# Kernel tuning notes

Hardware: AMD Instinct MI355X
Metric: run time of the kernel (lower is better)

## Reference

```python
import jax, jax.numpy as jnp
import numpy as np

DT = 0.1
EPS = 0.01


def _trans_layer(x, W, b):
    # x: [B, 2U]; W: [U, U]; b: [U]
    U = b.shape[0]
    t = DT / EPS
    u_in, v_in = x[:, :U], x[:, U:]
    act = jnp.tanh(u_in)
    v_star = (v_in + t * act) / (1.0 + t)
    # Block matrix A = [[I, dt*W], [-dt*W^T, I]] -- identical for all samples,
    # so factor/solve ONCE with a multi-RHS solve instead of torch's per-sample batched LU.
    I = jnp.eye(U, dtype=x.dtype)
    A = jnp.block([[I, DT * W], [-DT * W.T, I]])  # [2U, 2U]
    rhs = jnp.concatenate([u_in + DT * b, v_star], axis=1)  # [B, 2U]
    y = jnp.linalg.solve(A, rhs.T).T  # [B, 2U]
    u, v = y[:, :U], y[:, U:]
    u_out = DT * (v @ W.T) - u_in - DT * b
    v_out = -DT * (u @ W) + t * v - v_in - t * act
    return jnp.concatenate([u_out, v_out], axis=1)


def setup_inputs() -> dict:
    key = jax.random.key(0)
    ks = jax.random.split(key, 14)
    B, D_IN, U, D_OUT = 32768, 256, 256, 10

    def lin_w(k, o, i):
        return (jax.random.uniform(k, (o, i), jnp.float32) * 2.0 - 1.0) / np.sqrt(i).astype(np.float32)

    def lin_b(k, o, fan_in):
        return (jax.random.uniform(k, (o,), jnp.float32) * 2.0 - 1.0) / np.sqrt(fan_in).astype(np.float32)

    return {
        'x': jax.random.normal(ks[0], (B, D_IN), jnp.float32),
        'Wi': lin_w(ks[1], U, D_IN), 'bi': lin_b(ks[2], U, D_IN),
        'W1': lin_w(ks[3], U, U), 'b1': lin_b(ks[4], U, U),
        'W2': lin_w(ks[5], U, U), 'b2': lin_b(ks[6], U, U),
        'W3': lin_w(ks[7], U, U), 'b3': lin_b(ks[8], U, U),
        'W4': lin_w(ks[9], U, U), 'b4': lin_b(ks[10], U, U),
        'Wo': lin_w(ks[11], D_OUT, U), 'bo': lin_b(ks[12], D_OUT, U),
    }


def reference(x, Wi, bi, W1, b1, W2, b2, W3, b3, W4, b4, Wo, bo):
    U = W1.shape[0]
    z = x @ Wi.T + bi                       # linearInput
    z = jnp.concatenate([z, jnp.tanh(z)], axis=1)  # [B, 2U]
    for W, b in ((W1, b1), (W2, b2), (W3, b3), (W4, b4)):
        z = _trans_layer(z, W, b)
    z = z[:, :U]
    logits = z @ Wo.T + bo                  # linearOutput
    return jax.nn.softmax(logits, axis=1)
```

## Files before the change

### kernel.cpp

```cpp
#include <hip/hip_runtime.h>
#include <math.h>

#define DTC 0.1f

typedef _Float16 half8 __attribute__((ext_vector_type(8)));
typedef _Float16 half4v __attribute__((ext_vector_type(4)));
typedef float f32x4 __attribute__((ext_vector_type(4)));

__device__ __forceinline__ float fast_tanh(float x) {
  const float e = __expf(2.f * x);
  const float r = __builtin_amdgcn_rcpf(e + 1.f);
  return fmaf(-2.f, r, 1.f);
}


__global__ __launch_bounds__(256) void k_prep(
    const float* __restrict__ W0, const float* __restrict__ W1,
    const float* __restrict__ W2, const float* __restrict__ W3,
    const float* __restrict__ b2, const float* __restrict__ b3,
    const float* __restrict__ b4,
    _Float16* __restrict__ Wh, _Float16* __restrict__ Wt,
    float* __restrict__ crm) {
  const float* Ws[4] = {W0, W1, W2, W3};
  const int bid = blockIdx.x, tid = threadIdx.x;
  if (bid < 128) {
    const int t = bid * 256 + tid;
    const float* W = Ws[(t * 8) >> 16];
    const int off = (t * 8) & 65535;
    const float4 a = *(const float4*)&W[off];
    const float4 b = *(const float4*)&W[off + 4];
    half8 h;
    h[0] = (_Float16)a.x; h[1] = (_Float16)a.y; h[2] = (_Float16)a.z; h[3] = (_Float16)a.w;
    h[4] = (_Float16)b.x; h[5] = (_Float16)b.y; h[6] = (_Float16)b.z; h[7] = (_Float16)b.w;
    *(half8*)&Wh[t * 8] = h;
  } else if (bid < 384) {
    __shared__ float sh[32][33];
    const int b2i = bid - 128;
    const int l = b2i >> 6, t64 = b2i & 63;
    const int r0 = (t64 >> 3) * 32, c0 = (t64 & 7) * 32;
    const float* W = Ws[l];
    const int i = tid >> 5, j = tid & 31;
#pragma unroll
    for (int p = 0; p < 4; ++p)
      sh[p * 8 + i][j] = W[(r0 + p * 8 + i) * 256 + c0 + j];
    __syncthreads();
#pragma unroll
    for (int p = 0; p < 4; ++p)
      Wt[l * 65536 + (c0 + p * 8 + i) * 256 + r0 + j] = (_Float16)sh[j][p * 8 + i];
  } else {
    const int l = bid - 384;
    const float* W = Ws[l];
    const float* b = (l == 0) ? b2 : (l == 1) ? b3 : b4;
    float s = 0.f;
#pragma unroll 8
    for (int k = 0; k < 256; ++k) s = fmaf(b[k], W[k * 256 + tid], s);
    crm[l * 256 + tid] = -0.09f * s;
  }
}

__global__ __launch_bounds__(256) void k_smm3(const _Float16* __restrict__ A,
                                              const _Float16* __restrict__ B,
                                              const _Float16* __restrict__ Eadd,
                                              _Float16* __restrict__ C,
                                              float scale, int addI) {
  const int tid = threadIdx.x, wave = tid >> 6, lane = tid & 63;
  const int quad = lane >> 4, l16 = lane & 15;
  const int l = blockIdx.z;
  const _Float16* Al = A + (size_t)l * 65536;
  const _Float16* Bl = B + (size_t)l * 65536;
  _Float16* Cl = C + (size_t)l * 65536;
  const int m0 = blockIdx.y * 64 + wave * 16, n0 = blockIdx.x * 64;
  f32x4 acc[4] = {};
#pragma unroll
  for (int kt = 0; kt < 8; ++kt) {
    const half8 af = *(const half8*)&Al[(m0 + l16) * 256 + kt * 32 + quad * 8];
#pragma unroll
    for (int ni = 0; ni < 4; ++ni) {
      const half8 bf = *(const half8*)&Bl[(n0 + ni * 16 + l16) * 256 + kt * 32 + quad * 8];
      acc[ni] = __builtin_amdgcn_mfma_f32_16x16x32_f16(af, bf, acc[ni], 0, 0, 0);
    }
  }
#pragma unroll
  for (int ni = 0; ni < 4; ++ni)
#pragma unroll
    for (int r = 0; r < 4; ++r) {
      const int row = m0 + quad * 4 + r, col = n0 + ni * 16 + l16;
      float v = scale * acc[ni][r];
      if (addI) v += (row == col ? 1.f : 0.f) - (float)(Eadd + (size_t)l * 65536)[row * 256 + col];
      Cl[row * 256 + col] = (_Float16)v;
    }
}

__global__ __launch_bounds__(256) void k_pack(
    const _Float16* __restrict__ Ph, const _Float16* __restrict__ Qt,
    const _Float16* __restrict__ Wt, const float* __restrict__ Wi,
    const float* __restrict__ Wo,
    _Float16* __restrict__ PQP, _Float16* __restrict__ RmP,
    _Float16* __restrict__ WiP, _Float16* __restrict__ WoP) {
  const int t = blockIdx.x * 256 + threadIdx.x;
  if (t < 65536) {
    const int l = t >> 14, c = t & 16383;
    const int ntile = c >> 10, kt = (c >> 6) & 15, lb = c & 63;
    const int n = ntile * 16 + (lb & 15);
    const int kq = (lb >> 4) * 8;
    half8 h;
    if (kt < 8) {
      h = *(const half8*)&Ph[(size_t)l * 65536 + n * 256 + kt * 32 + kq];
#pragma unroll
      for (int j = 0; j < 8; ++j) h[j] = -h[j];
    } else {
      h = *(const half8*)&Qt[(size_t)l * 65536 + n * 256 + (kt - 8) * 32 + kq];
    }
    *(half8*)&PQP[(size_t)t * 8] = h;
  } else if (t < 90112) {
    const int tt = t - 65536;
    const int l = tt >> 13, c = tt & 8191;
    const int ntile = c >> 9, kt = (c >> 6) & 7, lb = c & 63;
    const int n = ntile * 16 + (lb & 15);
    const int k0 = kt * 32 + (lb >> 4) * 8;
    half8 h = *(const half8*)&Wt[(size_t)l * 65536 + n * 256 + k0];
#pragma unroll
    for (int j = 0; j < 8; ++j) h[j] = (_Float16)(-0.9f * (float)h[j]);
    *(half8*)&RmP[(size_t)tt * 8] = h;
  } else if (t < 98304) {
    const int c = t - 90112;
    const int ntile = c >> 9, kt = (c >> 6) & 7, lb = c & 63;
    const int n = ntile * 16 + (lb & 15);
    const int k0 = kt * 32 + (lb >> 4) * 8;
    const float4 a = *(const float4*)&Wi[n * 256 + k0];
    const float4 b = *(const float4*)&Wi[n * 256 + k0 + 4];
    half8 h;
    h[0] = (_Float16)a.x; h[1] = (_Float16)a.y; h[2] = (_Float16)a.z; h[3] = (_Float16)a.w;
    h[4] = (_Float16)b.x; h[5] = (_Float16)b.y; h[6] = (_Float16)b.z; h[7] = (_Float16)b.w;
    *(half8*)&WiP[(size_t)c * 8] = h;
  } else {
    const int c = t - 98304;
    const int kt = c >> 6, lb = c & 63;
    const int n = lb & 15;
    const int k0 = kt * 32 + (lb >> 4) * 8;
    half8 h;
#pragma unroll
    for (int j = 0; j < 8; ++j) h[j] = (_Float16)((n < 10) ? Wo[n * 256 + k0 + j] : 0.f);
    *(half8*)&WoP[(size_t)c * 8] = h;
  }
}


__device__ __forceinline__ void lds_w16h(_Float16* base, int row, int col, _Float16 v) {
  const int chunk = (col >> 3) ^ (row & 7);
  *(_Float16*)((char*)base + row * 512 + (chunk << 4) + (col & 7) * 2) = v;
}

template <int NKT, bool DUAL>
__device__ __forceinline__ void gemm_k(const _Float16* __restrict__ Bp,
                                       const _Float16* A1, const _Float16* A2,
                                       f32x4* acc, int wave, int lane, int quad, int l16) {
  half8 bf[3][2];
  auto loadB = [&](int kt, int s) {
#pragma unroll
    for (int ni = 0; ni < 2; ++ni)
      bf[s][ni] = *(const half8*)&Bp[(((wave * 2 + ni) * NKT + kt) * 64 + lane) * 8];
  };
  loadB(0, 0);
  loadB(1, 1);
#pragma unroll
  for (int kt = 0; kt < NKT; ++kt) {
    const int s = kt % 3;
    if (kt + 2 < NKT) loadB(kt + 2, (kt + 2) % 3);
    const _Float16* Ab = (DUAL && kt >= NKT / 2) ? A2 : A1;
    const int akt = DUAL ? (kt & (NKT / 2 - 1)) : kt;
    half8 af[4];
#pragma unroll
    for (int mi = 0; mi < 4; ++mi) {
      const int row = mi * 16 + l16;
      const int chunk = (akt * 4 + quad) ^ (row & 7);
      af[mi] = *(const half8*)((const char*)Ab + row * 512 + (chunk << 4));
    }
#pragma unroll
    for (int mi = 0; mi < 4; ++mi)
#pragma unroll
      for (int ni = 0; ni < 2; ++ni)
        acc[mi * 2 + ni] = __builtin_amdgcn_mfma_f32_16x16x32_f16(
            af[mi], bf[s][ni], acc[mi * 2 + ni], 0, 0, 0);
  }
}

__global__ __launch_bounds__(512, 4) void k_fused(
    const float* __restrict__ x, const _Float16* __restrict__ WiP,
    const _Float16* __restrict__ PQP, const _Float16* __restrict__ RmP,
    const _Float16* __restrict__ WoP, const float* __restrict__ bi,
    const float* __restrict__ b1, const float* __restrict__ b2,
    const float* __restrict__ b3, const float* __restrict__ b4,
    const float* __restrict__ crm, const float* __restrict__ bo,
    float* __restrict__ out) {
  __shared__ __align__(16) _Float16 A1[64 * 256];
  __shared__ __align__(16) _Float16 A2[64 * 256];
  const int tid = threadIdx.x;
  const int wave = tid >> 6, lane = tid & 63;
  const int quad = lane >> 4, l16 = lane & 15;
  const int m0 = blockIdx.x * 64;

#pragma unroll
  for (int it = 0; it < 8; ++it) {
    const int idx = it * 512 + tid;
    const int row = idx >> 6, c4 = idx & 63;
    const float4 v = *(const float4*)&x[(size_t)(m0 + row) * 256 + c4 * 4];
    const int chunk = (c4 >> 1) ^ (row & 7), part = c4 & 1;
    _Float16* p = (_Float16*)((char*)A1 + row * 512 + (chunk << 4) + (part << 3));
    p[0] = (_Float16)v.x; p[1] = (_Float16)v.y; p[2] = (_Float16)v.z; p[3] = (_Float16)v.w;
  }
  __syncthreads();

  f32x4 acc[8];
  const f32x4 zero = {0.f, 0.f, 0.f, 0.f};
  half4v uph[8], r2p[8];

#pragma unroll
  for (int t = 0; t < 8; ++t) acc[t] = zero;
  gemm_k<8, false>(WiP, A1, A1, acc, wave, lane, quad, l16);
  __syncthreads();
#pragma unroll
  for (int ni = 0; ni < 2; ++ni) {
    const int col = wave * 32 + ni * 16 + l16;
    const float bic = bi[col], b1c = DTC * b1[col];
#pragma unroll
    for (int mi = 0; mi < 4; ++mi) {
      half4v r2v;
#pragma unroll
      for (int r = 0; r < 4; ++r) {
        const float z = acc[mi * 2 + ni][r] + bic;
        const int row = mi * 16 + quad * 4 + r;
        lds_w16h(A1, row, col, (_Float16)(z + b1c));
        r2v[r] = (_Float16)fast_tanh(z);
        lds_w16h(A2, row, col, r2v[r]);
      }
      r2p[mi * 2 + ni] = r2v;
    }
  }
  __syncthreads();

#pragma unroll 1
  for (int l = 0; l < 4; ++l) {
#pragma unroll
    for (int t = 0; t < 8; ++t) acc[t] = zero;
    gemm_k<16, true>(PQP + (size_t)l * 131072, A1, A2, acc, wave, lane, quad, l16);
    __syncthreads();
    const float* bn = (l == 0) ? b2 : (l == 1) ? b3 : b4;
#pragma unroll
    for (int ni = 0; ni < 2; ++ni) {
      const int col = wave * 32 + ni * 16 + l16;
      const float bc = (l < 3) ? DTC * bn[col] : 0.f;
#pragma unroll
      for (int mi = 0; mi < 4; ++mi) {
        half4v uv;
#pragma unroll
        for (int r = 0; r < 4; ++r) {
          uv[r] = (_Float16)acc[mi * 2 + ni][r];
          lds_w16h(A1, mi * 16 + quad * 4 + r, col, (_Float16)(acc[mi * 2 + ni][r] + bc));
        }
        uph[mi * 2 + ni] = uv;
      }
    }
    __syncthreads();
    if (l < 3) {
#pragma unroll
      for (int t = 0; t < 8; ++t) acc[t] = zero;
      gemm_k<8, false>(RmP + (size_t)l * 65536, A1, A1, acc, wave, lane, quad, l16);
#pragma unroll
      for (int ni = 0; ni < 2; ++ni) {
        const int col = wave * 32 + ni * 16 + l16;
        const float cc = crm[l * 256 + col];
#pragma unroll
        for (int mi = 0; mi < 4; ++mi) {
          half4v nr2;
#pragma unroll
          for (int r = 0; r < 4; ++r) {
            const float vp = acc[mi * 2 + ni][r] - cc - (float)r2p[mi * 2 + ni][r];
            nr2[r] = (_Float16)((vp + 10.f * fast_tanh((float)uph[mi * 2 + ni][r])) * (1.f / 11.f));
            lds_w16h(A2, mi * 16 + quad * 4 + r, col, nr2[r]);
          }
          r2p[mi * 2 + ni] = nr2;
        }
      }
      __syncthreads();
    }
  }

  if (wave < 4) {
    f32x4 acch = zero;
#pragma unroll
    for (int kt = 0; kt < 8; ++kt) {
      const int row = wave * 16 + l16;
      const int chunk = (kt * 4 + quad) ^ (row & 7);
      const half8 af = *(const half8*)((const char*)A1 + row * 512 + (chunk << 4));
      const half8 bfr = *(const half8*)&WoP[(kt * 64 + lane) * 8];
      acch = __builtin_amdgcn_mfma_f32_16x16x32_f16(af, bfr, acch, 0, 0, 0);
    }
    const float bov = (l16 < 10) ? bo[l16] : -3.0e38f;
#pragma unroll
    for (int r = 0; r < 4; ++r) {
      float v = acch[r] + bov;
      float mx = v;
#pragma unroll
      for (int off = 1; off < 16; off <<= 1) mx = fmaxf(mx, __shfl_xor(mx, off, 64));
      const float e = __expf(v - mx);
      float s = e;
#pragma unroll
      for (int off = 1; off < 16; off <<= 1) s += __shfl_xor(s, off, 64);
      if (l16 < 10)
        out[(size_t)(m0 + wave * 16 + quad * 4 + r) * 10 + l16] = e * __builtin_amdgcn_rcpf(s);
    }
  }
}


extern "C" void kernel_launch(void* const* d_in, const int* in_sizes, int n_in,
                              void* d_out, int out_size, void* d_ws, size_t ws_size,
                              hipStream_t stream) {
  const float* x  = (const float*)d_in[0];
  const float* Wi = (const float*)d_in[1];
  const float* bi = (const float*)d_in[2];
  const float* W[4] = {(const float*)d_in[3], (const float*)d_in[5],
                       (const float*)d_in[7], (const float*)d_in[9]};
  const float* b[4] = {(const float*)d_in[4], (const float*)d_in[6],
                       (const float*)d_in[8], (const float*)d_in[10]};
  const float* Wo = (const float*)d_in[11];
  const float* bo = (const float*)d_in[12];
  float* out = (float*)d_out;

  const int Bsz = in_sizes[0] / 256;

  _Float16* hb = (_Float16*)d_ws;
  _Float16* WiP = hb;
  _Float16* WoP = hb + 65536;
  _Float16* PQP = hb + 69632;
  _Float16* RmP = hb + 593920;
  _Float16* Wh  = hb + 790528;
  _Float16* Wt  = hb + 1052672;
  _Float16* Eh  = hb + 1314816;
  _Float16* Ph  = hb + 1576960;
  _Float16* Qt  = hb + 1839104;
  float* crm = (float*)(hb + 2101248);

  const dim3 g64(4, 4, 4);
  k_prep<<<387, 256, 0, stream>>>(W[0], W[1], W[2], W[3], b[1], b[2], b[3],
                                  Wh, Wt, crm);
  k_smm3<<<g64, 256, 0, stream>>>(Wh, Wh, nullptr, Eh, 0.01f, 0);
  k_smm3<<<g64, 256, 0, stream>>>(Eh, Eh, Eh, Ph, 1.0f, 1);
  k_smm3<<<g64, 256, 0, stream>>>(Ph, Wt, nullptr, Qt, DTC, 0);
  k_pack<<<386, 256, 0, stream>>>(Ph, Qt, Wt, Wi, Wo, PQP, RmP, WiP, WoP);

  k_fused<<<Bsz / 64, 512, 0, stream>>>(x, WiP, PQP, RmP, WoP, bi,
                                        b[0], b[1], b[2], b[3], crm, bo, out);
}
```

Before: 222.7 us.

## Retile fused kernel to 32-row blocks with two waves owning 128 columns

The fused MLP kernel now processes 32 rows per block with 2 waves instead of 64 rows with 8 waves. Each wave computes a 32x128 output tile. It loads B fragments for 8 column tiles per k-step into registers, double-buffered across k-steps. The u and r2 intermediate state is no longer kept in registers; it is reread from LDS in the update step, which frees registers but adds LDS traffic and an extra barrier. Because blocks are smaller, each weight fragment is reused across fewer rows, so total L2 weight traffic roughly doubles.

```diff
diff --git a/kernel.cpp b/kernel.cpp
--- a/kernel.cpp
+++ b/kernel.cpp
@@ -150,42 +150,48 @@
   const int chunk = (col >> 3) ^ (row & 7);
   *(_Float16*)((char*)base + row * 512 + (chunk << 4) + (col & 7) * 2) = v;
 }
+__device__ __forceinline__ float lds_r16h(const _Float16* base, int row, int col) {
+  const int chunk = (col >> 3) ^ (row & 7);
+  return (float)*(const _Float16*)((const char*)base + row * 512 + (chunk << 4) + (col & 7) * 2);
+}
 
 template <int NKT, bool DUAL>
 __device__ __forceinline__ void gemm_k(const _Float16* __restrict__ Bp,
-                                       const _Float16* A1, const _Float16* A2,
-                                       f32x4* acc, int wave, int lane, int quad, int l16) {
-  half8 bf[3][2];
-  auto loadB = [&](int kt, int s) {
-#pragma unroll
-    for (int ni = 0; ni < 2; ++ni)
-      bf[s][ni] = *(const half8*)&Bp[(((wave * 2 + ni) * NKT + kt) * 64 + lane) * 8];
-  };
-  loadB(0, 0);
-  loadB(1, 1);
+                                       const _Float16* __restrict__ Aa,
+                                       const _Float16* __restrict__ Ab,
+                                       f32x4 (&acc)[16], int w, int lane,
+                                       int quad, int l16) {
+  half8 cb[8], nb[8];
+#pragma unroll
+  for (int ni = 0; ni < 8; ++ni)
+    cb[ni] = *(const half8*)&Bp[(size_t)(((w * 8 + ni) * NKT) * 64 + lane) * 8];
 #pragma unroll
   for (int kt = 0; kt < NKT; ++kt) {
-    const int s = kt % 3;
-    if (kt + 2 < NKT) loadB(kt + 2, (kt + 2) % 3);
-    const _Float16* Ab = (DUAL && kt >= NKT / 2) ? A2 : A1;
-    const int akt = DUAL ? (kt & (NKT / 2 - 1)) : kt;
-    half8 af[4];
-#pragma unroll
-    for (int mi = 0; mi < 4; ++mi) {
-      const int row = mi * 16 + l16;
-      const int chunk = (akt * 4 + quad) ^ (row & 7);
-      af[mi] = *(const half8*)((const char*)Ab + row * 512 + (chunk << 4));
-    }
-#pragma unroll
-    for (int mi = 0; mi < 4; ++mi)
-#pragma unroll
-      for (int ni = 0; ni < 2; ++ni)
-        acc[mi * 2 + ni] = __builtin_amdgcn_mfma_f32_16x16x32_f16(
-            af[mi], bf[s][ni], acc[mi * 2 + ni], 0, 0, 0);
-  }
-}
-
-__global__ __launch_bounds__(512, 4) void k_fused(
+    if (kt + 1 < NKT) {
+#pragma unroll
+      for (int ni = 0; ni < 8; ++ni)
+        nb[ni] = *(const half8*)&Bp[(size_t)(((w * 8 + ni) * NKT + kt + 1) * 64 + lane) * 8];
+    }
+    const _Float16* As = (DUAL && kt >= NKT / 2) ? Ab : Aa;
+    const int akt = DUAL ? (kt % (NKT / 2)) : kt;
+    const int r0 = l16, r1 = 16 + l16;
+    const half8 af0 = *(const half8*)((const char*)As + r0 * 512 +
+                                      (((akt * 4 + quad) ^ (r0 & 7)) << 4));
+    const half8 af1 = *(const half8*)((const char*)As + r1 * 512 +
+                                      (((akt * 4 + quad) ^ (r1 & 7)) << 4));
+#pragma unroll
+    for (int ni = 0; ni < 8; ++ni) {
+      acc[ni]     = __builtin_amdgcn_mfma_f32_16x16x32_f16(af0, cb[ni], acc[ni], 0, 0, 0);
+      acc[8 + ni] = __builtin_amdgcn_mfma_f32_16x16x32_f16(af1, cb[ni], acc[8 + ni], 0, 0, 0);
+    }
+    if (kt + 1 < NKT) {
+#pragma unroll
+      for (int ni = 0; ni < 8; ++ni) cb[ni] = nb[ni];
+    }
+  }
+}
+
+__global__ __launch_bounds__(128, 2) void k_fused(
     const float* __restrict__ x, const _Float16* __restrict__ WiP,
     const _Float16* __restrict__ PQP, const _Float16* __restrict__ RmP,
     const _Float16* __restrict__ WoP, const float* __restrict__ bi,
@@ -193,106 +199,96 @@
     const float* __restrict__ b3, const float* __restrict__ b4,
     const float* __restrict__ crm, const float* __restrict__ bo,
     float* __restrict__ out) {
-  __shared__ __align__(16) _Float16 A1[64 * 256];
-  __shared__ __align__(16) _Float16 A2[64 * 256];
+  __shared__ __align__(16) _Float16 R1[32 * 256];
+  __shared__ __align__(16) _Float16 R2[32 * 256];
   const int tid = threadIdx.x;
-  const int wave = tid >> 6, lane = tid & 63;
+  const int w = tid >> 6, lane = tid & 63;
   const int quad = lane >> 4, l16 = lane & 15;
-  const int m0 = blockIdx.x * 64;
-
-#pragma unroll
-  for (int it = 0; it < 8; ++it) {
-    const int idx = it * 512 + tid;
-    const int row = idx >> 6, c4 = idx & 63;
-    const float4 v = *(const float4*)&x[(size_t)(m0 + row) * 256 + c4 * 4];
-    const int chunk = (c4 >> 1) ^ (row & 7), part = c4 & 1;
-    _Float16* p = (_Float16*)((char*)A1 + row * 512 + (chunk << 4) + (part << 3));
+  const int m0 = blockIdx.x * 32;
+
+#pragma unroll
+  for (int it = 0; it < 16; ++it) {
+    const int row = w * 16 + it;
+    const float4 v = *(const float4*)&x[(size_t)(m0 + row) * 256 + lane * 4];
+    const int chunk = (lane >> 1) ^ (row & 7), part = lane & 1;
+    _Float16* p = (_Float16*)((char*)R1 + row * 512 + (chunk << 4) + (part << 3));
     p[0] = (_Float16)v.x; p[1] = (_Float16)v.y; p[2] = (_Float16)v.z; p[3] = (_Float16)v.w;
   }
   __syncthreads();
 
-  f32x4 acc[8];
+  f32x4 acc[16];
   const f32x4 zero = {0.f, 0.f, 0.f, 0.f};
-  half4v uph[8], r2p[8];
-
-#pragma unroll
-  for (int t = 0; t < 8; ++t) acc[t] = zero;
-  gemm_k<8, false>(WiP, A1, A1, acc, wave, lane, quad, l16);
+
+#pragma unroll
+  for (int t = 0; t < 16; ++t) acc[t] = zero;
+  gemm_k<8, false>(WiP, R1, R1, acc, w, lane, quad, l16);
   __syncthreads();
 #pragma unroll
-  for (int ni = 0; ni < 2; ++ni) {
-    const int col = wave * 32 + ni * 16 + l16;
+  for (int ni = 0; ni < 8; ++ni) {
+    const int col = w * 128 + ni * 16 + l16;
     const float bic = bi[col], b1c = DTC * b1[col];
 #pragma unroll
-    for (int mi = 0; mi < 4; ++mi) {
-      half4v r2v;
+    for (int mi = 0; mi < 2; ++mi)
 #pragma unroll
       for (int r = 0; r < 4; ++r) {
-        const float z = acc[mi * 2 + ni][r] + bic;
         const int row = mi * 16 + quad * 4 + r;
-        lds_w16h(A1, row, col, (_Float16)(z + b1c));
-        r2v[r] = (_Float16)fast_tanh(z);
-        lds_w16h(A2, row, col, r2v[r]);
+        const float z = acc[mi * 8 + ni][r] + bic;
+        lds_w16h(R1, row, col, (_Float16)(z + b1c));
+        lds_w16h(R2, row, col, (_Float16)fast_tanh(z));
       }
-      r2p[mi * 2 + ni] = r2v;
-    }
   }
   __syncthreads();
 
 #pragma unroll 1
   for (int l = 0; l < 4; ++l) {
 #pragma unroll
-    for (int t = 0; t < 8; ++t) acc[t] = zero;
-    gemm_k<16, true>(PQP + (size_t)l * 131072, A1, A2, acc, wave, lane, quad, l16);
+    for (int t = 0; t < 16; ++t) acc[t] = zero;
+    gemm_k<16, true>(PQP + (size_t)l * 131072, R1, R2, acc, w, lane, quad, l16);
     __syncthreads();
     const float* bn = (l == 0) ? b2 : (l == 1) ? b3 : b4;
 #pragma unroll
-    for (int ni = 0; ni < 2; ++ni) {
-      const int col = wave * 32 + ni * 16 + l16;
+    for (int ni = 0; ni < 8; ++ni) {
+      const int col = w * 128 + ni * 16 + l16;
       const float bc = (l < 3) ? DTC * bn[col] : 0.f;
 #pragma unroll
-      for (int mi = 0; mi < 4; ++mi) {
-        half4v uv;
-#pragma unroll
-        for (int r = 0; r < 4; ++r) {
-          uv[r] = (_Float16)acc[mi * 2 + ni][r];
-          lds_w16h(A1, mi * 16 + quad * 4 + r, col, (_Float16)(acc[mi * 2 + ni][r] + bc));
-        }
-        uph[mi * 2 + ni] = uv;
-      }
+      for (int mi = 0; mi < 2; ++mi)
+#pragma unroll
+        for (int r = 0; r < 4; ++r)
+          lds_w16h(R1, mi * 16 + quad * 4 + r, col, (_Float16)(acc[mi * 8 + ni][r] + bc));
     }
     __syncthreads();
     if (l < 3) {
 #pragma unroll
-      for (int t = 0; t < 8; ++t) acc[t] = zero;
-      gemm_k<8, false>(RmP + (size_t)l * 65536, A1, A1, acc, wave, lane, quad, l16);
-#pragma unroll
-      for (int ni = 0; ni < 2; ++ni) {
-        const int col = wave * 32 + ni * 16 + l16;
+      for (int t = 0; t < 16; ++t) acc[t] = zero;
+      gemm_k<8, false>(RmP + (size_t)l * 65536, R1, R1, acc, w, lane, quad, l16);
+      __syncthreads();
+#pragma unroll
+      for (int ni = 0; ni < 8; ++ni) {
+        const int col = w * 128 + ni * 16 + l16;
         const float cc = crm[l * 256 + col];
-#pragma unroll
-        for (int mi = 0; mi < 4; ++mi) {
-          half4v nr2;
+        const float bc = DTC * bn[col];
+#pragma unroll
+        for (int mi = 0; mi < 2; ++mi)
 #pragma unroll
           for (int r = 0; r < 4; ++r) {
-            const float vp = acc[mi * 2 + ni][r] - cc - (float)r2p[mi * 2 + ni][r];
-            nr2[r] = (_Float16)((vp + 10.f * fast_tanh((float)uph[mi * 2 + ni][r])) * (1.f / 11.f));
-            lds_w16h(A2, mi * 16 + quad * 4 + r, col, nr2[r]);
+            const int row = mi * 16 + quad * 4 + r;
+            const float uv = lds_r16h(R1, row, col) - bc;
+            const float r2o = lds_r16h(R2, row, col);
+            const float vp = acc[mi * 8 + ni][r] - cc - r2o;
+            lds_w16h(R2, row, col, (_Float16)((vp + 10.f * fast_tanh(uv)) * (1.f / 11.f)));
           }
-          r2p[mi * 2 + ni] = nr2;
-        }
       }
       __syncthreads();
     }
   }
 
-  if (wave < 4) {
+  {
     f32x4 acch = zero;
 #pragma unroll
     for (int kt = 0; kt < 8; ++kt) {
-      const int row = wave * 16 + l16;
+      const int row = w * 16 + l16;
       const int chunk = (kt * 4 + quad) ^ (row & 7);
-      const half8 af = *(const half8*)((const char*)A1 + row * 512 + (chunk << 4));
+      const half8 af = *(const half8*)((const char*)R1 + row * 512 + (chunk << 4));
       const half8 bfr = *(const half8*)&WoP[(kt * 64 + lane) * 8];
       acch = __builtin_amdgcn_mfma_f32_16x16x32_f16(af, bfr, acch, 0, 0, 0);
     }
@@ -308,7 +304,7 @@
 #pragma unroll
       for (int off = 1; off < 16; off <<= 1) s += __shfl_xor(s, off, 64);
       if (l16 < 10)
-        out[(size_t)(m0 + wave * 16 + quad * 4 + r) * 10 + l16] = e * __builtin_amdgcn_rcpf(s);
+        out[(size_t)(m0 + w * 16 + quad * 4 + r) * 10 + l16] = e * __builtin_amdgcn_rcpf(s);
     }
   }
 }
@@ -350,6 +346,6 @@
   k_smm3<<<g64, 256, 0, stream>>>(Ph, Wt, nullptr, Qt, DTC, 0);
   k_pack<<<386, 256, 0, stream>>>(Ph, Qt, Wt, Wi, Wo, PQP, RmP, WiP, WoP);
 
-  k_fused<<<Bsz / 64, 512, 0, stream>>>(x, WiP, PQP, RmP, WoP, bi,
+  k_fused<<<Bsz / 32, 128, 0, stream>>>(x, WiP, PQP, RmP, WoP, bi,
                                         b[0], b[1], b[2], b[3], crm, bo, out);
 }
```

After: 392.9 us. 1.76x slower.
